# Performance work log

Measured on AMD Instinct MI355X. Metric: run time of the kernel, lower is better.

## Reference

```python
import jax, jax.numpy as jnp
import numpy as np
from jax import lax

B, T, F, H, NC = 64, 256, 64, 128, 2


def setup_inputs() -> dict:
    key = jax.random.key(0)
    ks = jax.random.split(key, 10)
    # timestamps: sorted ints with duplicates -> exercises per-timestamp mean aggregation
    t = jnp.sort(jax.random.randint(ks[0], (B, T), 0, T // 2), axis=1).astype(jnp.float32)
    m = jax.random.randint(ks[1], (B, T), 0, F).astype(jnp.float32)
    x = jax.random.normal(ks[2], (B, T), dtype=jnp.float32)
    delt = jax.random.uniform(ks[3], (B, T), dtype=jnp.float32)
    X = jnp.stack([t, m, x, delt], axis=1)  # [B, 4, T]
    lengths = jax.random.randint(ks[4], (B,), T // 2, T + 1).astype(jnp.int32)
    s = 1.0 / np.sqrt(H + 1)
    W_lin = jax.random.uniform(ks[5], (F, H + 1, 4 * H), minval=-s, maxval=s, dtype=jnp.float32)
    b_lin = jax.random.uniform(ks[6], (F, 4 * H), minval=-s, maxval=s, dtype=jnp.float32)
    W_dec = jax.random.uniform(ks[7], (F,), minval=-1.0, maxval=1.0, dtype=jnp.float32)
    b_dec = jax.random.uniform(ks[8], (F,), minval=-1.0, maxval=1.0, dtype=jnp.float32)
    so = 1.0 / np.sqrt(F * H + H)
    k9, k10 = jax.random.split(ks[9])
    W_out = jax.random.uniform(k9, (F * H + H, NC), minval=-so, maxval=so, dtype=jnp.float32)
    b_out = jax.random.uniform(k10, (NC,), minval=-so, maxval=so, dtype=jnp.float32)
    return {"X": X, "lengths": lengths, "W_lin": W_lin, "b_lin": b_lin,
            "W_dec": W_dec, "b_dec": b_dec, "W_out": W_out, "b_out": b_out}


def _forward(X, lengths, W_lin, b_lin, W_dec, b_dec, W_out, b_out):
    nF, Hp1, H4 = W_lin.shape
    hs = Hp1 - 1
    t = X[:, 0]
    m = X[:, 1].astype(jnp.int32)
    x = X[:, 2]
    delt = X[:, 3]
    idx = jnp.arange(t.shape[1])
    valid = idx[None, :] < lengths[:, None]                       # event is real
    t_next = jnp.concatenate([t[:, 1:], t[:, -1:] + 1.0], axis=1)
    # last event of a consecutive-equal-timestamp group (within valid length)
    boundary = (idx[None, :] == (lengths[:, None] - 1)) | (t_next != t)

    def per_sample(m_s, x_s, d_s, v_s, b_s):
        def step(carry, inp):
            h_t, c_t, acc, cnt = carry
            mj, xj, dj, vj, bj = inp
            # feature-specific decay of that feature's hidden row
            dm = W_dec[mj] * dj + b_dec[mj]
            decay = jnp.exp(-jnp.maximum(0.0, dm))
            h_dec = decay * h_t[mj]
            inp_vec = jnp.concatenate([xj[None], h_dec])          # [H+1]
            gates = inp_vec @ W_lin[mj] + b_lin[mj]               # [4H]
            gi, gf, go, gc = jnp.split(gates, 4)
            c_cand = jax.nn.sigmoid(gf) * c_t + jax.nn.sigmoid(gi) * jnp.tanh(gc)
            h_row = jax.nn.sigmoid(go) * jnp.tanh(c_cand)
            h_t = jnp.where(vj, h_t.at[mj].set(h_row), h_t)
            acc = acc + jnp.where(vj, c_cand, 0.0)
            cnt = cnt + jnp.where(vj, 1.0, 0.0)
            close = vj & bj                                       # end of timestamp group
            c_t = jnp.where(close, acc / jnp.maximum(cnt, 1.0), c_t)
            acc = jnp.where(close, jnp.zeros_like(acc), acc)
            cnt = jnp.where(close, 0.0, cnt)
            return (h_t, c_t, acc, cnt), None

        init = (jnp.zeros((nF, hs), jnp.float32), jnp.zeros((hs,), jnp.float32),
                jnp.zeros((hs,), jnp.float32), jnp.float32(0.0))
        (h_t, c_t, _, _), _ = lax.scan(step, init, (m_s, x_s, d_s, v_s, b_s))
        feats = jnp.concatenate([c_t, h_t.reshape(-1)])           # [H + F*H]
        return jax.nn.softmax(feats @ W_out + b_out)

    return jax.vmap(per_sample)(m, x, delt, valid, boundary)      # [B, n_class]


def reference(X, lengths, W_lin, b_lin, W_dec, b_dec, W_out, b_out):
    return _forward(X, lengths, W_lin, b_lin, W_dec, b_dec, W_out, b_out)
```

## Files before the change

### kernel.cpp

```cpp
#include <hip/hip_runtime.h>
#include <math.h>

#define BATCH 64
#define T 256
#define NF 64
#define H 128
#define H4 512
#define HP1 129
#define WF_STRIDE (HP1 * H4)
#define FEATS (NF * H + H)
#define NTH 1024
#define PACK_UINT4_PER_F 8192
#define PACK_BYTES (64u * PACK_UINT4_PER_F * 16u)

typedef _Float16 half2_t __attribute__((ext_vector_type(2)));

__device__ __forceinline__ float sigmoidf_(float x) {
    return 1.0f / (1.0f + __expf(-x));
}

__device__ __forceinline__ float tanhf_(float x) {
    float ax = fabsf(x);
    float e = __expf(2.0f * ax);
    float r = 1.0f - 2.0f / (e + 1.0f);
    return copysignf(r, x);
}

__device__ __forceinline__ float fdot2_(half2_t a, half2_t b, float c) {
#if defined(__has_builtin)
#if __has_builtin(__builtin_amdgcn_fdot2)
    return __builtin_amdgcn_fdot2(a, b, c, false);
#else
    return fmaf((float)a.x, (float)b.x, fmaf((float)a.y, (float)b.y, c));
#endif
#else
    return fmaf((float)a.x, (float)b.x, fmaf((float)a.y, (float)b.y, c));
#endif
}

__global__ __launch_bounds__(256)
void repack_kernel(const float* __restrict__ W_lin, uint4* __restrict__ pack) {
    const int lin = blockIdx.x * 256 + threadIdx.x;
    const int f   = lin >> 13;
    const int i   = (lin >> 10) & 7;
    const int tid = lin & 1023;
    const int kh  = tid >> 9;
    const int c   = tid & 511;
    const int k0  = kh * 64 + i * 8;
    const float* src = W_lin + (size_t)f * WF_STRIDE + (size_t)(1 + k0) * H4 + c;
    half2_t h[4];
    #pragma unroll
    for (int r = 0; r < 4; ++r) {
        h[r].x = (_Float16)src[(2 * r) * H4];
        h[r].y = (_Float16)src[(2 * r + 1) * H4];
    }
    pack[lin] = *(uint4*)h;
}

__global__ __launch_bounds__(NTH, 4)
void lstm_scan_fp16_kernel(const float* __restrict__ X,
                           const int* __restrict__ lengths,
                           const float* __restrict__ W_lin,
                           const float* __restrict__ b_lin,
                           const float* __restrict__ W_dec,
                           const float* __restrict__ b_dec,
                           const float* __restrict__ W_out,
                           const float* __restrict__ b_out,
                           const uint4* __restrict__ pack,
                           float* __restrict__ out)
{
    __shared__ float s_feats[FEATS];
    __shared__ half2_t s_inp2[H / 2];
    __shared__ float s_part[2][H4];
    __shared__ float s_X[4 * T];
    __shared__ float s_wdec[NF];
    __shared__ float s_bdec[NF];
    __shared__ float s_red[32];

    float* s_ct = s_feats;
    float* s_ht = s_feats + H;

    const int tid = threadIdx.x;
    const int b   = blockIdx.x;
    const int c   = tid & 511;
    const int kh  = tid >> 9;

    const float* Xb = X + b * 4 * T;
    const int len = lengths[b];

    for (int i = tid; i < NF * H; i += NTH) s_ht[i] = 0.0f;
    for (int i = tid; i < 4 * T; i += NTH) s_X[i] = Xb[i];
    if (tid < NF) { s_wdec[tid] = W_dec[tid]; s_bdec[tid] = b_dec[tid]; }
    if (tid < H / 2) { half2_t z; z.x = (_Float16)0.0f; z.y = (_Float16)0.0f; s_inp2[tid] = z; }
    __syncthreads();

    float c_t = 0.0f, acc = 0.0f, cnt = 0.0f;

    uint4 bufA[8], bufB[8];
    float4 blA = make_float4(0.f, 0.f, 0.f, 0.f), blB = make_float4(0.f, 0.f, 0.f, 0.f);
    float  wxA = 0.0f, wxB = 0.0f;

    {
        const int m0 = (int)s_X[T];
        const uint4* Wp = pack + m0 * PACK_UINT4_PER_F + tid;
        #pragma unroll
        for (int i = 0; i < 8; ++i) bufA[i] = Wp[i * NTH];
        if (tid < H) {
            const float* bb = b_lin + m0 * H4 + tid;
            blA.x = bb[0]; blA.y = bb[H]; blA.z = bb[2 * H]; blA.w = bb[3 * H];
        }
        if (kh == 0) wxA = W_lin[(size_t)m0 * WF_STRIDE + c];
    }

    #define STEP(CURW, NXTW, CURB, NXTB, CURX, NXTX)                                \
    {                                                                               \
        const int   mj = (int)s_X[T + j];                                           \
        const float xj = s_X[2 * T + j];                                            \
        const int   jn = (j + 1 < T) ? (j + 1) : (T - 1);                           \
        const int   mjn = (int)s_X[T + jn];                                         \
              \
        {                                                                           \
            const uint4* Wp = pack + mjn * PACK_UINT4_PER_F + tid;                  \
            _Pragma("unroll")                                                       \
            for (int i = 0; i < 8; ++i) NXTW[i] = Wp[i * NTH];                      \
        }                                                                           \
        if (tid < H) {                                                              \
            const float* bb = b_lin + mjn * H4 + tid;                               \
            NXTB.x = bb[0]; NXTB.y = bb[H]; NXTB.z = bb[2 * H]; NXTB.w = bb[3 * H]; \
        }                                                                           \
        if (kh == 0) NXTX = W_lin[(size_t)mjn * WF_STRIDE + c];                     \
                                     \
        float a0 = 0.0f, a1 = 0.0f;                                                 \
        _Pragma("unroll")                                                           \
        for (int i = 0; i < 8; ++i) {                                               \
            union { uint4 u; half2_t h[4]; } cv;                                    \
            cv.u = CURW[i];                                                         \
            const int ib = (kh << 5) + (i << 2);                                    \
            a0 = fdot2_(cv.h[0], s_inp2[ib],     a0);                               \
            a1 = fdot2_(cv.h[1], s_inp2[ib + 1], a1);                               \
            a0 = fdot2_(cv.h[2], s_inp2[ib + 2], a0);                               \
            a1 = fdot2_(cv.h[3], s_inp2[ib + 3], a1);                               \
        }                                                                           \
        float a = a0 + a1;                                                          \
        if (kh == 0) a = fmaf(xj, CURX, a);                                         \
        s_part[kh][c] = a;                                                          \
        __syncthreads();                                     \
        if (tid < H) {                                                              \
            const int h = tid;                                                      \
            const float gi = s_part[0][h]       + s_part[1][h]       + CURB.x;      \
            const float gf = s_part[0][H + h]   + s_part[1][H + h]   + CURB.y;      \
            const float go = s_part[0][2*H + h] + s_part[1][2*H + h] + CURB.z;      \
            const float gc = s_part[0][3*H + h] + s_part[1][3*H + h] + CURB.w;      \
            const float c_cand = sigmoidf_(gf) * c_t + sigmoidf_(gi) * tanhf_(gc);  \
            const float h_row  = sigmoidf_(go) * tanhf_(c_cand);                    \
            s_ht[mj * H + h] = h_row;                                               \
            acc += c_cand;                                                          \
            cnt += 1.0f;                                                            \
            const float tj = s_X[j];                                                \
            const float tn = (j < T - 1) ? s_X[j + 1] : (tj + 1.0f);                \
            const bool boundary = (j == len - 1) || (tn != tj);                     \
            if (boundary) { c_t = acc / fmaxf(cnt, 1.0f); acc = 0.0f; cnt = 0.0f; } \
                                      \
            const float dn  = s_X[3 * T + jn];                                      \
            const float dmn = fmaf(s_wdec[mjn], dn, s_bdec[mjn]);                   \
            const float den = __expf(-fmaxf(0.0f, dmn));                            \
            const float hv  = (mjn == mj) ? h_row : s_ht[mjn * H + h];              \
            ((_Float16*)s_inp2)[h] = (_Float16)(den * hv);                          \
        }                                                                           \
        __syncthreads();                                 \
    }

    int j = 0;
    while (j < len) {
        STEP(bufA, bufB, blA, blB, wxA, wxB); ++j;
        if (j >= len) break;
        STEP(bufB, bufA, blB, blA, wxB, wxA); ++j;
    }
    #undef STEP

    if (tid < H) s_ct[tid] = c_t;
    __syncthreads();

    float z0 = 0.0f, z1 = 0.0f;
    for (int i = tid; i < FEATS; i += NTH) {
        const float f = s_feats[i];
        const float2 w = *(const float2*)(W_out + 2 * i);
        z0 = fmaf(f, w.x, z0);
        z1 = fmaf(f, w.y, z1);
    }
    #pragma unroll
    for (int off = 32; off > 0; off >>= 1) {
        z0 += __shfl_down(z0, off, 64);
        z1 += __shfl_down(z1, off, 64);
    }
    const int wave = tid >> 6, lane = tid & 63;
    if (lane == 0) { s_red[2 * wave] = z0; s_red[2 * wave + 1] = z1; }
    __syncthreads();
    if (tid == 0) {
        float a0 = b_out[0], a1 = b_out[1];
        #pragma unroll
        for (int w = 0; w < 16; ++w) { a0 += s_red[2 * w]; a1 += s_red[2 * w + 1]; }
        const float mx = fmaxf(a0, a1);
        const float e0 = __expf(a0 - mx), e1 = __expf(a1 - mx);
        const float inv = 1.0f / (e0 + e1);
        out[2 * b]     = e0 * inv;
        out[2 * b + 1] = e1 * inv;
    }
}

#define NTHREADS 512
__global__ __launch_bounds__(NTHREADS)
void lstm_scan_kernel(const float* __restrict__ X,
                      const int* __restrict__ lengths,
                      const float* __restrict__ W_lin,
                      const float* __restrict__ b_lin,
                      const float* __restrict__ W_dec,
                      const float* __restrict__ b_dec,
                      const float* __restrict__ W_out,
                      const float* __restrict__ b_out,
                      float* __restrict__ out)
{
    __shared__ float s_feats[FEATS];
    __shared__ float s_inp[H];
    __shared__ float s_part[4][H4];
    __shared__ float s_X[4 * T];
    __shared__ float s_wdec[NF];
    __shared__ float s_bdec[NF];
    __shared__ float s_red[16];

    float* s_ct = s_feats;
    float* s_ht = s_feats + H;

    const int tid = threadIdx.x;
    const int b   = blockIdx.x;
    const int g4  = tid & 127;
    const int kq  = tid >> 7;

    const float* Xb = X + b * 4 * T;
    const int len = lengths[b];

    for (int i = tid; i < NF * H; i += NTHREADS) s_ht[i] = 0.0f;
    for (int i = tid; i < 4 * T; i += NTHREADS) s_X[i] = Xb[i];
    if (tid < NF) { s_wdec[tid] = W_dec[tid]; s_bdec[tid] = b_dec[tid]; }
    __syncthreads();

    float c_t = 0.0f, acc = 0.0f, cnt = 0.0f;

    for (int j = 0; j < len; ++j) {
        const int   mj = (int)s_X[T + j];
        const float xj = s_X[2 * T + j];
        const float* Wf = W_lin + mj * WF_STRIDE;

        float bl0, bl1, bl2, bl3;
        if (tid < H) {
            const float dj    = s_X[3 * T + j];
            const float dm    = fmaf(s_wdec[mj], dj, s_bdec[mj]);
            const float decay = __expf(-fmaxf(0.0f, dm));
            s_inp[tid] = decay * s_ht[mj * H + tid];
            const int m4 = mj * H4;
            bl0 = b_lin[m4 + tid];
            bl1 = b_lin[m4 + H + tid];
            bl2 = b_lin[m4 + 2 * H + tid];
            bl3 = b_lin[m4 + 3 * H + tid];
        }
        __syncthreads();

        float4 a4 = make_float4(0.0f, 0.0f, 0.0f, 0.0f);
        {
            const float*  wr  = Wf + (1 + kq * 32) * H4 + 4 * g4;
            const float4* ivp = (const float4*)(s_inp + kq * 32);
            #pragma unroll
            for (int c = 0; c < 8; ++c) {
                const float4 v = ivp[c];
                const float* wrc = wr + (4 * c) * H4;
                const float4 w0 = *(const float4*)(wrc);
                const float4 w1 = *(const float4*)(wrc + H4);
                const float4 w2 = *(const float4*)(wrc + 2 * H4);
                const float4 w3 = *(const float4*)(wrc + 3 * H4);
                a4.x = fmaf(v.x, w0.x, a4.x); a4.y = fmaf(v.x, w0.y, a4.y);
                a4.z = fmaf(v.x, w0.z, a4.z); a4.w = fmaf(v.x, w0.w, a4.w);
                a4.x = fmaf(v.y, w1.x, a4.x); a4.y = fmaf(v.y, w1.y, a4.y);
                a4.z = fmaf(v.y, w1.z, a4.z); a4.w = fmaf(v.y, w1.w, a4.w);
                a4.x = fmaf(v.z, w2.x, a4.x); a4.y = fmaf(v.z, w2.y, a4.y);
                a4.z = fmaf(v.z, w2.z, a4.z); a4.w = fmaf(v.z, w2.w, a4.w);
                a4.x = fmaf(v.w, w3.x, a4.x); a4.y = fmaf(v.w, w3.y, a4.y);
                a4.z = fmaf(v.w, w3.z, a4.z); a4.w = fmaf(v.w, w3.w, a4.w);
            }
        }
        if (kq == 0) {
            const float4 w = *(const float4*)(Wf + 4 * g4);
            a4.x = fmaf(xj, w.x, a4.x); a4.y = fmaf(xj, w.y, a4.y);
            a4.z = fmaf(xj, w.z, a4.z); a4.w = fmaf(xj, w.w, a4.w);
        }
        *(float4*)(&s_part[kq][4 * g4]) = a4;
        __syncthreads();

        if (tid < H) {
            const int h = tid;
            const float gi = s_part[0][h]         + s_part[1][h]         + s_part[2][h]         + s_part[3][h]         + bl0;
            const float gf = s_part[0][H + h]     + s_part[1][H + h]     + s_part[2][H + h]     + s_part[3][H + h]     + bl1;
            const float go = s_part[0][2*H + h]   + s_part[1][2*H + h]   + s_part[2][2*H + h]   + s_part[3][2*H + h]   + bl2;
            const float gc = s_part[0][3*H + h]   + s_part[1][3*H + h]   + s_part[2][3*H + h]   + s_part[3][3*H + h]   + bl3;

            const float c_cand = sigmoidf_(gf) * c_t + sigmoidf_(gi) * tanhf_(gc);
            const float h_row  = sigmoidf_(go) * tanhf_(c_cand);
            s_ht[mj * H + h] = h_row;
            acc += c_cand;
            cnt += 1.0f;

            const float tj = s_X[j];
            const float tn = (j < T - 1) ? s_X[j + 1] : (tj + 1.0f);
            const bool boundary = (j == len - 1) || (tn != tj);
            if (boundary) { c_t = acc / fmaxf(cnt, 1.0f); acc = 0.0f; cnt = 0.0f; }
        }
        __syncthreads();
    }

    if (tid < H) s_ct[tid] = c_t;
    __syncthreads();

    float z0 = 0.0f, z1 = 0.0f;
    for (int i = tid; i < FEATS; i += NTHREADS) {
        const float f = s_feats[i];
        const float2 w = *(const float2*)(W_out + 2 * i);
        z0 = fmaf(f, w.x, z0);
        z1 = fmaf(f, w.y, z1);
    }
    #pragma unroll
    for (int off = 32; off > 0; off >>= 1) {
        z0 += __shfl_down(z0, off, 64);
        z1 += __shfl_down(z1, off, 64);
    }
    const int wave = tid >> 6, lane = tid & 63;
    if (lane == 0) { s_red[2 * wave] = z0; s_red[2 * wave + 1] = z1; }
    __syncthreads();
    if (tid == 0) {
        float a0 = b_out[0], a1 = b_out[1];
        #pragma unroll
        for (int w = 0; w < 8; ++w) { a0 += s_red[2 * w]; a1 += s_red[2 * w + 1]; }
        const float mx = fmaxf(a0, a1);
        const float e0 = __expf(a0 - mx), e1 = __expf(a1 - mx);
        const float inv = 1.0f / (e0 + e1);
        out[2 * b]     = e0 * inv;
        out[2 * b + 1] = e1 * inv;
    }
}

extern "C" void kernel_launch(void* const* d_in, const int* in_sizes, int n_in,
                              void* d_out, int out_size, void* d_ws, size_t ws_size,
                              hipStream_t stream) {
    const float* X      = (const float*)d_in[0];
    const int*   lens   = (const int*)d_in[1];
    const float* W_lin  = (const float*)d_in[2];
    const float* b_lin  = (const float*)d_in[3];
    const float* W_dec  = (const float*)d_in[4];
    const float* b_dec  = (const float*)d_in[5];
    const float* W_out  = (const float*)d_in[6];
    const float* b_out  = (const float*)d_in[7];
    float* out = (float*)d_out;

    if (ws_size >= (size_t)PACK_BYTES) {
        uint4* pack = (uint4*)d_ws;
        hipLaunchKernelGGL(repack_kernel, dim3(2048), dim3(256), 0, stream, W_lin, pack);
        hipLaunchKernelGGL(lstm_scan_fp16_kernel, dim3(BATCH), dim3(NTH), 0, stream,
                           X, lens, W_lin, b_lin, W_dec, b_dec, W_out, b_out, pack, out);
    } else {
        hipLaunchKernelGGL(lstm_scan_kernel, dim3(BATCH), dim3(NTHREADS), 0, stream,
                           X, lens, W_lin, b_lin, W_dec, b_dec, W_out, b_out, out);
    }
}
```

Measured before the change: 500.2 us.

## Stream fp16 LSTM weights into LDS via async global_load_lds triple buffering

Replaces the register double-buffered weight prefetch with direct global-to-LDS DMA (global_load_lds) across a 3-slot chunk ring. Each step's 128x512 weight slab is split into four chunks that are consumed while the next ones are still being fetched. The x-column weights and the biases are also packed into an fp16 header that is DMA'd per step. The goal is to cut register pressure and hide per-step global load latency. The cost is two extra preprocessing launches, fp16 rounding of the biases, reliance on hand-written waitcnt and barrier sequences, and roughly 100KB of LDS per block.

```diff
diff --git a/kernel.cpp b/kernel.cpp
--- a/kernel.cpp
+++ b/kernel.cpp
@@ -1,5 +1,6 @@
 #include <hip/hip_runtime.h>
 #include <math.h>
+#include <stdint.h>
 
 #define BATCH 64
 #define T 256
@@ -10,8 +11,12 @@
 #define WF_STRIDE (HP1 * H4)
 #define FEATS (NF * H + H)
 #define NTH 1024
-#define PACK_UINT4_PER_F 8192
-#define PACK_BYTES (64u * PACK_UINT4_PER_F * 16u)
+
+#define CHUNK_BYTES 32768
+#define PACK_U4_PER_F 8192
+#define PACK_BYTES (64u * PACK_U4_PER_F * 16u)
+#define HDR_BYTES  (64u * 1024u * 2u)
+#define WS_NEED ((size_t)HDR_BYTES + (size_t)PACK_BYTES)
 
 typedef _Float16 half2_t __attribute__((ext_vector_type(2)));
 
@@ -38,15 +43,46 @@
 #endif
 }
 
+#if defined(__has_builtin)
+#if __has_builtin(__builtin_amdgcn_global_load_lds)
+#define HAVE_GLL 1
+#endif
+#endif
+
+__device__ __forceinline__ void dma16(const void* g, uint32_t lds_byte) {
+#ifdef HAVE_GLL
+    __builtin_amdgcn_global_load_lds(
+        (const __attribute__((address_space(1))) void*)g,
+        (__attribute__((address_space(3))) void*)(uintptr_t)lds_byte,
+        16, 0, 0);
+#endif
+}
+__device__ __forceinline__ void dma4(const void* g, uint32_t lds_byte) {
+#ifdef HAVE_GLL
+    __builtin_amdgcn_global_load_lds(
+        (const __attribute__((address_space(1))) void*)g,
+        (__attribute__((address_space(3))) void*)(uintptr_t)lds_byte,
+        4, 0, 0);
+#endif
+}
+
+#define WAITV(N) do { asm volatile("s_waitcnt vmcnt(" #N ")" ::: "memory"); \
+                      __builtin_amdgcn_sched_barrier(0); } while (0)
+#define BARRIER() do { asm volatile("s_waitcnt lgkmcnt(0)" ::: "memory"); \
+                       __builtin_amdgcn_s_barrier(); \
+                       asm volatile("" ::: "memory"); } while (0)
+
 __global__ __launch_bounds__(256)
 void repack_kernel(const float* __restrict__ W_lin, uint4* __restrict__ pack) {
     const int lin = blockIdx.x * 256 + threadIdx.x;
     const int f   = lin >> 13;
-    const int i   = (lin >> 10) & 7;
-    const int tid = lin & 1023;
+    const int idx = lin & 8191;
+    const int tid = idx & 1023;
+    const int i   = (idx >> 10) & 1;
+    const int cc  = idx >> 11;
     const int kh  = tid >> 9;
     const int c   = tid & 511;
-    const int k0  = kh * 64 + i * 8;
+    const int k0  = cc * 32 + kh * 16 + i * 8;
     const float* src = W_lin + (size_t)f * WF_STRIDE + (size_t)(1 + k0) * H4 + c;
     half2_t h[4];
     #pragma unroll
@@ -57,33 +93,43 @@
     pack[lin] = *(uint4*)h;
 }
 
+__global__ __launch_bounds__(256)
+void hdr_kernel(const float* __restrict__ W_lin, const float* __restrict__ b_lin,
+                _Float16* __restrict__ hdr) {
+    const int lin = blockIdx.x * 256 + threadIdx.x;
+    const int f = lin >> 10, t = lin & 1023;
+    const float v = (t < 512) ? W_lin[(size_t)f * WF_STRIDE + t]
+                              : b_lin[f * H4 + (t & 511)];
+    hdr[lin] = (_Float16)v;
+}
+
 __global__ __launch_bounds__(NTH, 4)
-void lstm_scan_fp16_kernel(const float* __restrict__ X,
-                           const int* __restrict__ lengths,
-                           const float* __restrict__ W_lin,
-                           const float* __restrict__ b_lin,
-                           const float* __restrict__ W_dec,
-                           const float* __restrict__ b_dec,
-                           const float* __restrict__ W_out,
-                           const float* __restrict__ b_out,
-                           const uint4* __restrict__ pack,
-                           float* __restrict__ out)
+void lstm_scan_dma(const float* __restrict__ X,
+                   const int* __restrict__ lengths,
+                   const float* __restrict__ W_dec,
+                   const float* __restrict__ b_dec,
+                   const float* __restrict__ W_out,
+                   const float* __restrict__ b_out,
+                   const uint4* __restrict__ pack,
+                   const _Float16* __restrict__ hdr,
+                   float* __restrict__ out)
 {
-    __shared__ float s_feats[FEATS];
-    __shared__ half2_t s_inp2[H / 2];
+    __shared__ __align__(16) char s_wb[3 * CHUNK_BYTES];
+    __shared__ __align__(16) char s_hdr[2 * 4096];
+    __shared__ __align__(16) char s_inp2[64 * 4];
+    __shared__ float s_ht[NF * H];
     __shared__ float s_part[2][H4];
     __shared__ float s_X[4 * T];
     __shared__ float s_wdec[NF];
     __shared__ float s_bdec[NF];
+    __shared__ float s_cfin[H];
     __shared__ float s_red[32];
-
-    float* s_ct = s_feats;
-    float* s_ht = s_feats + H;
 
     const int tid = threadIdx.x;
     const int b   = blockIdx.x;
+    const int wv  = tid >> 6;
+    const int kh  = tid >> 9;
     const int c   = tid & 511;
-    const int kh  = tid >> 9;
 
     const float* Xb = X + b * 4 * T;
     const int len = lengths[b];
@@ -91,99 +137,116 @@
     for (int i = tid; i < NF * H; i += NTH) s_ht[i] = 0.0f;
     for (int i = tid; i < 4 * T; i += NTH) s_X[i] = Xb[i];
     if (tid < NF) { s_wdec[tid] = W_dec[tid]; s_bdec[tid] = b_dec[tid]; }
-    if (tid < H / 2) { half2_t z; z.x = (_Float16)0.0f; z.y = (_Float16)0.0f; s_inp2[tid] = z; }
-    __syncthreads();
+    if (tid < H) ((_Float16*)s_inp2)[tid] = (_Float16)0.0f;
+    __syncthreads();
+
+    const uint32_t wb_base  = (uint32_t)(uintptr_t)s_wb;
+    const uint32_t hd_base  = (uint32_t)(uintptr_t)s_hdr;
+    const uint32_t wb_st = __builtin_amdgcn_readfirstlane(wb_base + wv * 1024);
+    const uint32_t hd_st = __builtin_amdgcn_readfirstlane(hd_base + wv * 256);
+    const uint32_t wb_rd = wb_base + tid * 16;
 
     float c_t = 0.0f, acc = 0.0f, cnt = 0.0f;
 
-    uint4 bufA[8], bufB[8];
-    float4 blA = make_float4(0.f, 0.f, 0.f, 0.f), blB = make_float4(0.f, 0.f, 0.f, 0.f);
-    float  wxA = 0.0f, wxB = 0.0f;
+    #define STAGE_W(fv, ccv, OFF) do {                                          \
+        const uint4* gp = pack + (size_t)(((fv) * 4 + (ccv)) * 2) * 1024 + tid; \
+        dma16(gp,        wb_st + (OFF));                                        \
+        dma16(gp + 1024, wb_st + (OFF) + 16384);                                \
+    } while (0)
+
+    #define STAGE_H(sv) do {                                                    \
+        const int ss = ((sv) < T) ? (sv) : (T - 1);                             \
+        const _Float16* gh = hdr + (int)s_X[T + ss] * 1024 + (tid & 1022);      \
+        dma4(gh, hd_st + (((sv) & 1) ? 4096 : 0));                              \
+    } while (0)
+
+    #define CHUNK_C(ccv, OFF) do {                                              \
+        uint4 w0, w1;                                                           \
+        const uint32_t ra = wb_rd + (OFF);                                      \
+        asm volatile("ds_read_b128 %0, %2 offset:0\n\t"                         \
+                     "ds_read_b128 %1, %2 offset:16384"                         \
+                     : "=&v"(w0), "=&v"(w1) : "v"(ra) : "memory");              \
+        const uint4 iv0 = *(const uint4*)(s_inp2 + ((ccv) * 16 + kh * 8) * 4);  \
+        const uint4 iv1 = *(const uint4*)(s_inp2 + ((ccv) * 16 + kh * 8 + 4) * 4); \
+        asm volatile("s_waitcnt lgkmcnt(0)" ::: "memory");                      \
+        __builtin_amdgcn_sched_barrier(0);                                      \
+        union { uint4 u; half2_t h[4]; } cw0, cw1, ci0, ci1;                    \
+        cw0.u = w0; cw1.u = w1; ci0.u = iv0; ci1.u = iv1;                       \
+        a0 = fdot2_(cw0.h[0], ci0.h[0], a0); a1 = fdot2_(cw0.h[1], ci0.h[1], a1); \
+        a0 = fdot2_(cw0.h[2], ci0.h[2], a0); a1 = fdot2_(cw0.h[3], ci0.h[3], a1); \
+        a0 = fdot2_(cw1.h[0], ci1.h[0], a0); a1 = fdot2_(cw1.h[1], ci1.h[1], a1); \
+        a0 = fdot2_(cw1.h[2], ci1.h[2], a0); a1 = fdot2_(cw1.h[3], ci1.h[3], a1); \
+    } while (0)
 
     {
         const int m0 = (int)s_X[T];
-        const uint4* Wp = pack + m0 * PACK_UINT4_PER_F + tid;
-        #pragma unroll
-        for (int i = 0; i < 8; ++i) bufA[i] = Wp[i * NTH];
-        if (tid < H) {
-            const float* bb = b_lin + m0 * H4 + tid;
-            blA.x = bb[0]; blA.y = bb[H]; blA.z = bb[2 * H]; blA.w = bb[3 * H];
-        }
-        if (kh == 0) wxA = W_lin[(size_t)m0 * WF_STRIDE + c];
-    }
-
-    #define STEP(CURW, NXTW, CURB, NXTB, CURX, NXTX)                                \
-    {                                                                               \
-        const int   mj = (int)s_X[T + j];                                           \
-        const float xj = s_X[2 * T + j];                                            \
-        const int   jn = (j + 1 < T) ? (j + 1) : (T - 1);                           \
-        const int   mjn = (int)s_X[T + jn];                                         \
-              \
-        {                                                                           \
-            const uint4* Wp = pack + mjn * PACK_UINT4_PER_F + tid;                  \
-            _Pragma("unroll")                                                       \
-            for (int i = 0; i < 8; ++i) NXTW[i] = Wp[i * NTH];                      \
-        }                                                                           \
-        if (tid < H) {                                                              \
-            const float* bb = b_lin + mjn * H4 + tid;                               \
-            NXTB.x = bb[0]; NXTB.y = bb[H]; NXTB.z = bb[2 * H]; NXTB.w = bb[3 * H]; \
-        }                                                                           \
-        if (kh == 0) NXTX = W_lin[(size_t)mjn * WF_STRIDE + c];                     \
-                                     \
-        float a0 = 0.0f, a1 = 0.0f;                                                 \
-        _Pragma("unroll")                                                           \
-        for (int i = 0; i < 8; ++i) {                                               \
-            union { uint4 u; half2_t h[4]; } cv;                                    \
-            cv.u = CURW[i];                                                         \
-            const int ib = (kh << 5) + (i << 2);                                    \
-            a0 = fdot2_(cv.h[0], s_inp2[ib],     a0);                               \
-            a1 = fdot2_(cv.h[1], s_inp2[ib + 1], a1);                               \
-            a0 = fdot2_(cv.h[2], s_inp2[ib + 2], a0);                               \
-            a1 = fdot2_(cv.h[3], s_inp2[ib + 3], a1);                               \
-        }                                                                           \
-        float a = a0 + a1;                                                          \
-        if (kh == 0) a = fmaf(xj, CURX, a);                                         \
-        s_part[kh][c] = a;                                                          \
-        __syncthreads();                                     \
-        if (tid < H) {                                                              \
-            const int h = tid;                                                      \
-            const float gi = s_part[0][h]       + s_part[1][h]       + CURB.x;      \
-            const float gf = s_part[0][H + h]   + s_part[1][H + h]   + CURB.y;      \
-            const float go = s_part[0][2*H + h] + s_part[1][2*H + h] + CURB.z;      \
-            const float gc = s_part[0][3*H + h] + s_part[1][3*H + h] + CURB.w;      \
-            const float c_cand = sigmoidf_(gf) * c_t + sigmoidf_(gi) * tanhf_(gc);  \
-            const float h_row  = sigmoidf_(go) * tanhf_(c_cand);                    \
-            s_ht[mj * H + h] = h_row;                                               \
-            acc += c_cand;                                                          \
-            cnt += 1.0f;                                                            \
-            const float tj = s_X[j];                                                \
-            const float tn = (j < T - 1) ? s_X[j + 1] : (tj + 1.0f);                \
-            const bool boundary = (j == len - 1) || (tn != tj);                     \
+        STAGE_W(m0, 0, 0);
+        STAGE_W(m0, 1, CHUNK_BYTES);
+        STAGE_H(0);
+    }
+
+    #define STEP(O0, O1, O2) {                                                  \
+        const int   mj  = (int)s_X[T + j];                                      \
+        const float xj  = s_X[2 * T + j];                                       \
+        const int   jn  = (j + 1 < T) ? (j + 1) : (T - 1);                      \
+        const int   mjn = (int)s_X[T + jn];                                     \
+        float a0 = 0.0f, a1 = 0.0f;                                             \
+        STAGE_W(mj, 2, O2);  STAGE_H(j + 1); WAITV(5); CHUNK_C(0, O0);          \
+        STAGE_W(mj, 3, O0);                  WAITV(5); CHUNK_C(1, O1);          \
+        STAGE_W(mjn, 0, O1);                 WAITV(5); CHUNK_C(2, O2);          \
+        STAGE_W(mjn, 1, O2);                 WAITV(4); CHUNK_C(3, O0);          \
+        float a = a0 + a1;                                                      \
+        {                                                                       \
+            const float hv = (float)*(const _Float16*)(s_hdr                    \
+                + ((j & 1) ? 4096 : 0) + tid * 4 + (tid & 1) * 2);              \
+            a = kh ? (a + hv) : fmaf(xj, hv, a);                                \
+        }                                                                       \
+        s_part[kh][c] = a;                                                      \
+        BARRIER();                                          \
+        if (tid < H) {                                                          \
+            const int h = tid;                                                  \
+            const float gi = s_part[0][h]         + s_part[1][h];               \
+            const float gf = s_part[0][H + h]     + s_part[1][H + h];           \
+            const float go = s_part[0][2 * H + h] + s_part[1][2 * H + h];       \
+            const float gc = s_part[0][3 * H + h] + s_part[1][3 * H + h];       \
+            const float c_cand = sigmoidf_(gf) * c_t + sigmoidf_(gi) * tanhf_(gc); \
+            const float h_row  = sigmoidf_(go) * tanhf_(c_cand);                \
+            s_ht[mj * H + h] = h_row;                                           \
+            acc += c_cand;                                                      \
+            cnt += 1.0f;                                                        \
+            const float tj = s_X[j];                                            \
+            const float tn = (j < T - 1) ? s_X[j + 1] : (tj + 1.0f);            \
+            const bool boundary = (j == len - 1) || (tn != tj);                 \
             if (boundary) { c_t = acc / fmaxf(cnt, 1.0f); acc = 0.0f; cnt = 0.0f; } \
-                                      \
-            const float dn  = s_X[3 * T + jn];                                      \
-            const float dmn = fmaf(s_wdec[mjn], dn, s_bdec[mjn]);                   \
-            const float den = __expf(-fmaxf(0.0f, dmn));                            \
-            const float hv  = (mjn == mj) ? h_row : s_ht[mjn * H + h];              \
-            ((_Float16*)s_inp2)[h] = (_Float16)(den * hv);                          \
-        }                                                                           \
-        __syncthreads();                                 \
+            const float dn  = s_X[3 * T + jn];                                  \
+            const float dmn = fmaf(s_wdec[mjn], dn, s_bdec[mjn]);               \
+            const float den = __expf(-fmaxf(0.0f, dmn));                        \
+            const float hv2 = (mjn == mj) ? h_row : s_ht[mjn * H + h];          \
+            ((_Float16*)s_inp2)[h] = (_Float16)(den * hv2);                     \
+        }                                                                       \
+        BARRIER();                                      \
     }
 
     int j = 0;
-    while (j < len) {
-        STEP(bufA, bufB, blA, blB, wxA, wxB); ++j;
-        if (j >= len) break;
-        STEP(bufB, bufA, blB, blA, wxB, wxA); ++j;
+    for (;;) {
+        STEP(0, CHUNK_BYTES, 2 * CHUNK_BYTES); ++j; if (j >= len) break;
+        STEP(CHUNK_BYTES, 2 * CHUNK_BYTES, 0); ++j; if (j >= len) break;
+        STEP(2 * CHUNK_BYTES, 0, CHUNK_BYTES); ++j; if (j >= len) break;
     }
     #undef STEP
-
-    if (tid < H) s_ct[tid] = c_t;
+    #undef CHUNK_C
+    #undef STAGE_W
+    #undef STAGE_H
+
+    asm volatile("s_waitcnt vmcnt(0) lgkmcnt(0)" ::: "memory");
+    __syncthreads();
+
+    if (tid < H) s_cfin[tid] = c_t;
     __syncthreads();
 
     float z0 = 0.0f, z1 = 0.0f;
     for (int i = tid; i < FEATS; i += NTH) {
-        const float f = s_feats[i];
+        const float f = (i < H) ? s_cfin[i] : s_ht[i - H];
         const float2 w = *(const float2*)(W_out + 2 * i);
         z0 = fmaf(f, w.x, z0);
         z1 = fmaf(f, w.y, z1);
@@ -270,9 +333,9 @@
             const float*  wr  = Wf + (1 + kq * 32) * H4 + 4 * g4;
             const float4* ivp = (const float4*)(s_inp + kq * 32);
             #pragma unroll
-            for (int c = 0; c < 8; ++c) {
-                const float4 v = ivp[c];
-                const float* wrc = wr + (4 * c) * H4;
+            for (int cc = 0; cc < 8; ++cc) {
+                const float4 v = ivp[cc];
+                const float* wrc = wr + (4 * cc) * H4;
                 const float4 w0 = *(const float4*)(wrc);
                 const float4 w1 = *(const float4*)(wrc + H4);
                 const float4 w2 = *(const float4*)(wrc + 2 * H4);
@@ -359,11 +422,13 @@
     const float* b_out  = (const float*)d_in[7];
     float* out = (float*)d_out;
 
-    if (ws_size >= (size_t)PACK_BYTES) {
-        uint4* pack = (uint4*)d_ws;
+    if (ws_size >= WS_NEED) {
+        _Float16* hdr = (_Float16*)d_ws;
+        uint4* pack = (uint4*)((char*)d_ws + HDR_BYTES);
         hipLaunchKernelGGL(repack_kernel, dim3(2048), dim3(256), 0, stream, W_lin, pack);
-        hipLaunchKernelGGL(lstm_scan_fp16_kernel, dim3(BATCH), dim3(NTH), 0, stream,
-                           X, lens, W_lin, b_lin, W_dec, b_dec, W_out, b_out, pack, out);
+        hipLaunchKernelGGL(hdr_kernel, dim3(256), dim3(256), 0, stream, W_lin, b_lin, hdr);
+        hipLaunchKernelGGL(lstm_scan_dma, dim3(BATCH), dim3(NTH), 0, stream,
+                           X, lens, W_dec, b_dec, W_out, b_out, pack, hdr, out);
     } else {
         hipLaunchKernelGGL(lstm_scan_kernel, dim3(BATCH), dim3(NTHREADS), 0, stream,
                            X, lens, W_lin, b_lin, W_dec, b_dec, W_out, b_out, out);
```

New measurement: 587.2 us. +17.4%, slower.

## Quantize recurrent LSTM weights to FP8 with scaled packing and split prefetch

Applied to the files above, without the earlier changes.

Repacks the per-feature recurrent weight matrix into FP8 (pre-scaled by 4096) instead of FP16, halving the bytes streamed per timestep, and decodes them to half2 for fdot2 accumulation. The prefetch is split: the first half of the K dimension is double-buffered for the next event, while the second half is loaded on demand within the current step. This lowers memory traffic in the latency-bound sequential scan, at the cost of extra conversion instructions, a partly unprefetched load, and reduced weight precision that may exceed accuracy tolerances.

```diff
diff --git a/kernel.cpp b/kernel.cpp
--- a/kernel.cpp
+++ b/kernel.cpp
@@ -1,5 +1,6 @@
 #include <hip/hip_runtime.h>
 #include <math.h>
+#include <stdint.h>
 
 #define BATCH 64
 #define T 256
@@ -10,10 +11,12 @@
 #define WF_STRIDE (HP1 * H4)
 #define FEATS (NF * H + H)
 #define NTH 1024
-#define PACK_UINT4_PER_F 8192
-#define PACK_BYTES (64u * PACK_UINT4_PER_F * 16u)
+
+#define PACK8_U4 (64 * 2 * 2 * 1024)
+#define PACK8_BYTES ((size_t)PACK8_U4 * 16u)
 
 typedef _Float16 half2_t __attribute__((ext_vector_type(2)));
+typedef float    vf2     __attribute__((ext_vector_type(2)));
 
 __device__ __forceinline__ float sigmoidf_(float x) {
     return 1.0f / (1.0f + __expf(-x));
@@ -38,36 +41,50 @@
 #endif
 }
 
+template<bool HI>
+__device__ __forceinline__ half2_t dec8(unsigned u) {
+    vf2 f = __builtin_amdgcn_cvt_pk_f32_fp8(u, HI);
+    return (half2_t)__builtin_amdgcn_cvt_pkrtz(f[0], f[1]);
+}
+
 __global__ __launch_bounds__(256)
-void repack_kernel(const float* __restrict__ W_lin, uint4* __restrict__ pack) {
+void repack8_kernel(const float* __restrict__ W_lin, uint4* __restrict__ pack) {
     const int lin = blockIdx.x * 256 + threadIdx.x;
-    const int f   = lin >> 13;
-    const int i   = (lin >> 10) & 7;
     const int tid = lin & 1023;
+    const int q   = (lin >> 10) & 1;
+    const int h   = (lin >> 11) & 1;
+    const int f   = lin >> 12;
     const int kh  = tid >> 9;
-    const int c   = tid & 511;
-    const int k0  = kh * 64 + i * 8;
-    const float* src = W_lin + (size_t)f * WF_STRIDE + (size_t)(1 + k0) * H4 + c;
-    half2_t h[4];
+    const int cc  = tid & 511;
+    const int k0  = h * 64 + kh * 32 + q * 16;
+    const float* src = W_lin + (size_t)f * WF_STRIDE + (size_t)(1 + k0) * H4 + cc;
+    unsigned u[4];
     #pragma unroll
-    for (int r = 0; r < 4; ++r) {
-        h[r].x = (_Float16)src[(2 * r) * H4];
-        h[r].y = (_Float16)src[(2 * r + 1) * H4];
-    }
-    pack[lin] = *(uint4*)h;
+    for (int w = 0; w < 4; ++w) {
+        const float v0 = src[(4 * w + 0) * H4] * 4096.0f;
+        const float v1 = src[(4 * w + 1) * H4] * 4096.0f;
+        const float v2 = src[(4 * w + 2) * H4] * 4096.0f;
+        const float v3 = src[(4 * w + 3) * H4] * 4096.0f;
+        unsigned r = 0;
+        r = __builtin_amdgcn_cvt_pk_fp8_f32(v0, v1, r, false);
+        r = __builtin_amdgcn_cvt_pk_fp8_f32(v2, v3, r, true);
+        u[w] = r;
+    }
+    uint4 o; o.x = u[0]; o.y = u[1]; o.z = u[2]; o.w = u[3];
+    pack[lin] = o;
 }
 
 __global__ __launch_bounds__(NTH, 4)
-void lstm_scan_fp16_kernel(const float* __restrict__ X,
-                           const int* __restrict__ lengths,
-                           const float* __restrict__ W_lin,
-                           const float* __restrict__ b_lin,
-                           const float* __restrict__ W_dec,
-                           const float* __restrict__ b_dec,
-                           const float* __restrict__ W_out,
-                           const float* __restrict__ b_out,
-                           const uint4* __restrict__ pack,
-                           float* __restrict__ out)
+void lstm_scan_fp8_kernel(const float* __restrict__ X,
+                          const int* __restrict__ lengths,
+                          const float* __restrict__ W_lin,
+                          const float* __restrict__ b_lin,
+                          const float* __restrict__ W_dec,
+                          const float* __restrict__ b_dec,
+                          const float* __restrict__ W_out,
+                          const float* __restrict__ b_out,
+                          const uint4* __restrict__ pack,
+                          float* __restrict__ out)
 {
     __shared__ float s_feats[FEATS];
     __shared__ half2_t s_inp2[H / 2];
@@ -96,15 +113,29 @@
 
     float c_t = 0.0f, acc = 0.0f, cnt = 0.0f;
 
-    uint4 bufA[8], bufB[8];
+    #define DOTU4(W, IB) do {                                                   \
+        const half2_t* ip = ((const half2_t*)s_inp2) + (IB);                    \
+        union { uint4 u; half2_t h[4]; } I0, I1;                                \
+        I0.u = *(const uint4*)(ip);                                             \
+        I1.u = *(const uint4*)(ip + 4);                                         \
+        a = fdot2_(dec8<false>(W.x), I0.h[0], a);                               \
+        a = fdot2_(dec8<true >(W.x), I0.h[1], a);                               \
+        a = fdot2_(dec8<false>(W.y), I0.h[2], a);                               \
+        a = fdot2_(dec8<true >(W.y), I0.h[3], a);                               \
+        a = fdot2_(dec8<false>(W.z), I1.h[0], a);                               \
+        a = fdot2_(dec8<true >(W.z), I1.h[1], a);                               \
+        a = fdot2_(dec8<false>(W.w), I1.h[2], a);                               \
+        a = fdot2_(dec8<true >(W.w), I1.h[3], a);                               \
+    } while (0)
+
+    uint4 A0a, A0b, B0a, B0b;
     float4 blA = make_float4(0.f, 0.f, 0.f, 0.f), blB = make_float4(0.f, 0.f, 0.f, 0.f);
     float  wxA = 0.0f, wxB = 0.0f;
 
     {
         const int m0 = (int)s_X[T];
-        const uint4* Wp = pack + m0 * PACK_UINT4_PER_F + tid;
-        #pragma unroll
-        for (int i = 0; i < 8; ++i) bufA[i] = Wp[i * NTH];
+        const uint4* p0 = pack + (size_t)(m0 * 2) * 2048;
+        A0a = p0[tid]; A0b = p0[1024 + tid];
         if (tid < H) {
             const float* bb = b_lin + m0 * H4 + tid;
             blA.x = bb[0]; blA.y = bb[H]; blA.z = bb[2 * H]; blA.w = bb[3 * H];
@@ -112,71 +143,67 @@
         if (kh == 0) wxA = W_lin[(size_t)m0 * WF_STRIDE + c];
     }
 
-    #define STEP(CURW, NXTW, CURB, NXTB, CURX, NXTX)                                \
-    {                                                                               \
-        const int   mj = (int)s_X[T + j];                                           \
-        const float xj = s_X[2 * T + j];                                            \
-        const int   jn = (j + 1 < T) ? (j + 1) : (T - 1);                           \
-        const int   mjn = (int)s_X[T + jn];                                         \
-              \
-        {                                                                           \
-            const uint4* Wp = pack + mjn * PACK_UINT4_PER_F + tid;                  \
-            _Pragma("unroll")                                                       \
-            for (int i = 0; i < 8; ++i) NXTW[i] = Wp[i * NTH];                      \
-        }                                                                           \
-        if (tid < H) {                                                              \
-            const float* bb = b_lin + mjn * H4 + tid;                               \
-            NXTB.x = bb[0]; NXTB.y = bb[H]; NXTB.z = bb[2 * H]; NXTB.w = bb[3 * H]; \
-        }                                                                           \
-        if (kh == 0) NXTX = W_lin[(size_t)mjn * WF_STRIDE + c];                     \
-                                     \
-        float a0 = 0.0f, a1 = 0.0f;                                                 \
-        _Pragma("unroll")                                                           \
-        for (int i = 0; i < 8; ++i) {                                               \
-            union { uint4 u; half2_t h[4]; } cv;                                    \
-            cv.u = CURW[i];                                                         \
-            const int ib = (kh << 5) + (i << 2);                                    \
-            a0 = fdot2_(cv.h[0], s_inp2[ib],     a0);                               \
-            a1 = fdot2_(cv.h[1], s_inp2[ib + 1], a1);                               \
-            a0 = fdot2_(cv.h[2], s_inp2[ib + 2], a0);                               \
-            a1 = fdot2_(cv.h[3], s_inp2[ib + 3], a1);                               \
-        }                                                                           \
-        float a = a0 + a1;                                                          \
-        if (kh == 0) a = fmaf(xj, CURX, a);                                         \
-        s_part[kh][c] = a;                                                          \
-        __syncthreads();                                     \
-        if (tid < H) {                                                              \
-            const int h = tid;                                                      \
-            const float gi = s_part[0][h]       + s_part[1][h]       + CURB.x;      \
-            const float gf = s_part[0][H + h]   + s_part[1][H + h]   + CURB.y;      \
-            const float go = s_part[0][2*H + h] + s_part[1][2*H + h] + CURB.z;      \
-            const float gc = s_part[0][3*H + h] + s_part[1][3*H + h] + CURB.w;      \
-            const float c_cand = sigmoidf_(gf) * c_t + sigmoidf_(gi) * tanhf_(gc);  \
-            const float h_row  = sigmoidf_(go) * tanhf_(c_cand);                    \
-            s_ht[mj * H + h] = h_row;                                               \
-            acc += c_cand;                                                          \
-            cnt += 1.0f;                                                            \
-            const float tj = s_X[j];                                                \
-            const float tn = (j < T - 1) ? s_X[j + 1] : (tj + 1.0f);                \
-            const bool boundary = (j == len - 1) || (tn != tj);                     \
+    #define STEP(C0A, C0B, N0A, N0B, CBL, NBL, CWX, NWX)                        \
+    {                                                                           \
+        const int   mj  = (int)s_X[T + j];                                      \
+        const float xj  = s_X[2 * T + j];                                       \
+        const int   jn  = (j + 1 < T) ? (j + 1) : (T - 1);                      \
+        const int   mjn = (int)s_X[T + jn];                                     \
+                                                 \
+        const uint4* p1 = pack + (size_t)(mj * 2 + 1) * 2048;                   \
+        const uint4 h1a = p1[tid];                                              \
+        const uint4 h1b = p1[1024 + tid];                                       \
+                            \
+        const uint4* p0n = pack + (size_t)(mjn * 2) * 2048;                     \
+        N0A = p0n[tid]; N0B = p0n[1024 + tid];                                  \
+        if (tid < H) {                                                          \
+            const float* bb = b_lin + mjn * H4 + tid;                           \
+            NBL.x = bb[0]; NBL.y = bb[H]; NBL.z = bb[2 * H]; NBL.w = bb[3 * H]; \
+        }                                                                       \
+        if (kh == 0) NWX = W_lin[(size_t)mjn * WF_STRIDE + c];                  \
+               \
+        float a = 0.0f;                                                         \
+        DOTU4(C0A, kh * 16);                                                    \
+        DOTU4(C0B, kh * 16 + 8);                                                \
+        DOTU4(h1a, 32 + kh * 16);                                               \
+        DOTU4(h1b, 32 + kh * 16 + 8);                                           \
+        a *= (1.0f / 4096.0f);                                                  \
+        if (kh == 0) a = fmaf(xj, CWX, a);                                      \
+        s_part[kh][c] = a;                                                      \
+        __syncthreads();                                 \
+        if (tid < H) {                                                          \
+            const int h = tid;                                                  \
+            const float gi = s_part[0][h]       + s_part[1][h]       + CBL.x;   \
+            const float gf = s_part[0][H + h]   + s_part[1][H + h]   + CBL.y;   \
+            const float go = s_part[0][2*H + h] + s_part[1][2*H + h] + CBL.z;   \
+            const float gc = s_part[0][3*H + h] + s_part[1][3*H + h] + CBL.w;   \
+            const float c_cand = sigmoidf_(gf) * c_t + sigmoidf_(gi) * tanhf_(gc); \
+            const float h_row  = sigmoidf_(go) * tanhf_(c_cand);                \
+            s_ht[mj * H + h] = h_row;                                           \
+            acc += c_cand;                                                      \
+            cnt += 1.0f;                                                        \
+            const float tj = s_X[j];                                            \
+            const float tn = (j < T - 1) ? s_X[j + 1] : (tj + 1.0f);            \
+            const bool boundary = (j == len - 1) || (tn != tj);                 \
             if (boundary) { c_t = acc / fmaxf(cnt, 1.0f); acc = 0.0f; cnt = 0.0f; } \
-                                      \
-            const float dn  = s_X[3 * T + jn];                                      \
-            const float dmn = fmaf(s_wdec[mjn], dn, s_bdec[mjn]);                   \
-            const float den = __expf(-fmaxf(0.0f, dmn));                            \
-            const float hv  = (mjn == mj) ? h_row : s_ht[mjn * H + h];              \
-            ((_Float16*)s_inp2)[h] = (_Float16)(den * hv);                          \
-        }                                                                           \
-        __syncthreads();                                 \
+                                  \
+            const float dn  = s_X[3 * T + jn];                                  \
+            const float dmn = fmaf(s_wdec[mjn], dn, s_bdec[mjn]);               \
+            const float den = __expf(-fmaxf(0.0f, dmn));                        \
+            const float hv  = (mjn == mj) ? h_row : s_ht[mjn * H + h];          \
+            ((_Float16*)s_inp2)[h] = (_Float16)(den * hv);                      \
+        }                                                                       \
+        __syncthreads();                             \
     }
 
     int j = 0;
     while (j < len) {
-        STEP(bufA, bufB, blA, blB, wxA, wxB); ++j;
+        STEP(A0a, A0b, B0a, B0b, blA, blB, wxA, wxB); ++j;
         if (j >= len) break;
-        STEP(bufB, bufA, blB, blA, wxB, wxA); ++j;
+        STEP(B0a, B0b, A0a, A0b, blB, blA, wxB, wxA); ++j;
     }
     #undef STEP
+    #undef DOTU4
 
     if (tid < H) s_ct[tid] = c_t;
     __syncthreads();
@@ -270,9 +297,9 @@
             const float*  wr  = Wf + (1 + kq * 32) * H4 + 4 * g4;
             const float4* ivp = (const float4*)(s_inp + kq * 32);
             #pragma unroll
-            for (int c = 0; c < 8; ++c) {
-                const float4 v = ivp[c];
-                const float* wrc = wr + (4 * c) * H4;
+            for (int cc = 0; cc < 8; ++cc) {
+                const float4 v = ivp[cc];
+                const float* wrc = wr + (4 * cc) * H4;
                 const float4 w0 = *(const float4*)(wrc);
                 const float4 w1 = *(const float4*)(wrc + H4);
                 const float4 w2 = *(const float4*)(wrc + 2 * H4);
@@ -359,10 +386,11 @@
     const float* b_out  = (const float*)d_in[7];
     float* out = (float*)d_out;
 
-    if (ws_size >= (size_t)PACK_BYTES) {
+    if (ws_size >= PACK8_BYTES) {
         uint4* pack = (uint4*)d_ws;
-        hipLaunchKernelGGL(repack_kernel, dim3(2048), dim3(256), 0, stream, W_lin, pack);
-        hipLaunchKernelGGL(lstm_scan_fp16_kernel, dim3(BATCH), dim3(NTH), 0, stream,
+        hipLaunchKernelGGL(repack8_kernel, dim3(PACK8_U4 / 256), dim3(256), 0, stream,
+                           W_lin, pack);
+        hipLaunchKernelGGL(lstm_scan_fp8_kernel, dim3(BATCH), dim3(NTH), 0, stream,
                            X, lens, W_lin, b_lin, W_dec, b_dec, W_out, b_out, pack, out);
     } else {
         hipLaunchKernelGGL(lstm_scan_kernel, dim3(BATCH), dim3(NTHREADS), 0, stream,
```

Result: faster. 465.7 us (-6.9%).
